# Kernel tuning notes

Measured on AMD Instinct MI355X. Metric: run time of the kernel, lower is better.

## Reference

```python
import jax, jax.numpy as jnp
import numpy as np
from jax.ops import segment_sum, segment_max

N_NODES, N_EDGES, D_IN, D_H, D_E, HEADS, LAYERS, D_OUT, N_GRAPHS = 50000, 150000, 48, 64, 16, 10, 3, 128, 4096


def setup_inputs() -> dict:
    key = jax.random.key(0)
    ks = jax.random.split(key, 24)
    x = jax.random.normal(ks[0], (N_NODES, D_IN), jnp.float32)
    edge_attr = jax.random.uniform(ks[1], (N_EDGES, D_E), jnp.float32)
    edge_index = jax.random.randint(ks[2], (2, N_EDGES), 0, N_NODES, dtype=jnp.int32)
    batch_ids = jnp.sort(jax.random.randint(ks[3], (N_NODES,), 0, N_GRAPHS, dtype=jnp.int32))
    s = 0.05
    W_emb = jax.random.normal(ks[4], (D_IN, D_H), jnp.float32) * s
    b_emb = jnp.zeros((D_H,), jnp.float32)
    Ws = jax.random.normal(ks[5], (LAYERS, D_H, HEADS * D_H), jnp.float32) * s
    att_src = jax.random.normal(ks[6], (LAYERS, HEADS, D_H), jnp.float32) * s
    att_dst = jax.random.normal(ks[7], (LAYERS, HEADS, D_H), jnp.float32) * s
    att_edge = jax.random.normal(ks[8], (LAYERS, HEADS, D_H), jnp.float32) * s
    W_edge = jax.random.normal(ks[9], (LAYERS, D_E, HEADS * D_H), jnp.float32) * s
    bias = jnp.zeros((LAYERS, D_H), jnp.float32)
    bn_gamma = jnp.ones((LAYERS, D_H), jnp.float32)
    bn_beta = jnp.zeros((LAYERS, D_H), jnp.float32)
    bn_mean = jax.random.normal(ks[10], (LAYERS, D_H), jnp.float32) * 0.1
    bn_var = jax.random.uniform(ks[11], (LAYERS, D_H), jnp.float32) + 0.5
    W_out = jax.random.normal(ks[12], (D_H, D_OUT), jnp.float32) * s
    b_out = jnp.zeros((D_OUT,), jnp.float32)
    return dict(x=x, edge_attr=edge_attr, W_emb=W_emb, b_emb=b_emb, Ws=Ws,
                att_src=att_src, att_dst=att_dst, att_edge=att_edge, W_edge=W_edge,
                bias=bias, bn_gamma=bn_gamma, bn_beta=bn_beta, bn_mean=bn_mean,
                bn_var=bn_var, W_out=W_out, b_out=b_out,
                edge_index=edge_index, batch_ids=batch_ids)


def reference(x, edge_attr, W_emb, b_emb, Ws, att_src, att_dst, att_edge, W_edge,
              bias, bn_gamma, bn_beta, bn_mean, bn_var, W_out, b_out,
              edge_index, batch_ids):
    N = x.shape[0]
    H, F = att_src.shape[1], att_src.shape[2]
    src, dst = edge_index[0], edge_index[1]
    # PyG add_self_loops(fill_value='mean'): self-loop edge_attr = scatter-mean of incoming edge_attr
    cnt = segment_sum(jnp.ones(src.shape, jnp.float32), dst, num_segments=N)
    loop_attr = segment_sum(edge_attr, dst, num_segments=N) / jnp.maximum(cnt, 1.0)[:, None]
    ar = jnp.arange(N, dtype=src.dtype)
    src2 = jnp.concatenate([src, ar])
    dst2 = jnp.concatenate([dst, ar])
    ea2 = jnp.concatenate([edge_attr, loop_attr], axis=0)  # [E+N, De]

    h = x @ W_emb + b_emb  # [N, D_H]
    for i in range(Ws.shape[0]):
        xp = (h @ Ws[i]).reshape(N, H, F)                       # [N,H,F]
        a_s = jnp.einsum('nhf,hf->nh', xp, att_src[i])
        a_d = jnp.einsum('nhf,hf->nh', xp, att_dst[i])
        ep = (ea2 @ W_edge[i]).reshape(-1, H, F)                # [E2,H,F]
        a_e = jnp.einsum('ehf,hf->eh', ep, att_edge[i])
        alpha = jax.nn.leaky_relu(a_s[src2] + a_d[dst2] + a_e, 0.2)  # [E2,H]
        m = segment_max(alpha, dst2, num_segments=N)            # segment softmax over dst
        e = jnp.exp(alpha - m[dst2])
        z = segment_sum(e, dst2, num_segments=N)
        att = e / z[dst2]                                       # [E2,H]
        agg = segment_sum(xp[src2] * att[:, :, None], dst2, num_segments=N)  # [N,H,F]
        xc = agg.mean(axis=1) + bias[i]                         # concat=False -> head mean
        xc = (xc - bn_mean[i]) * bn_gamma[i] / jnp.sqrt(bn_var[i] + 1e-5) + bn_beta[i]
        xc = jax.nn.gelu(xc, approximate=False)
        h = h + xc                                              # residual_connection == 'res'
    out = h @ W_out + b_out                                     # [N, D_OUT]
    gsum = segment_sum(out, batch_ids, num_segments=N_GRAPHS)
    gcnt = segment_sum(jnp.ones((N,), jnp.float32), batch_ids, num_segments=N_GRAPHS)
    return gsum / jnp.maximum(gcnt, 1.0)[:, None]               # global_mean_pool [G, D_OUT]
```

## Files before the change

### kernel.cpp

```cpp
#include <hip/hip_runtime.h>
#include <hip/hip_fp16.h>
#include <math.h>

constexpr int NN   = 50000;
constexpr int NE   = 150000;
constexpr int DIN  = 48;
constexpr int DH   = 64;
constexpr int DE   = 16;
constexpr int NHD  = 10;
constexpr int NL   = 3;
constexpr int DOUTC= 128;
constexpr int NG   = 4096;
constexpr int E2   = NE + NN;
constexpr int SCAN_B  = 256;
constexpr int SCAN_NB = (NN + SCAN_B - 1) / SCAN_B;

typedef __bf16 v8bf __attribute__((ext_vector_type(8)));
typedef short  v8s  __attribute__((ext_vector_type(8)));
typedef float  v4f  __attribute__((ext_vector_type(4)));

__device__ inline unsigned short f2bf(float f) {
    unsigned u = __builtin_bit_cast(unsigned, f);
    unsigned r = (u + 0x7FFFu + ((u >> 16) & 1u)) >> 16;
    return (unsigned short)r;
}

__device__ inline v4f MF(v8s a, v8s b, v4f c) {
    return __builtin_amdgcn_mfma_f32_16x16x32_bf16(
        __builtin_bit_cast(v8bf, a), __builtin_bit_cast(v8bf, b), c, 0, 0, 0);
}
__device__ inline v4f MFB(v8bf a, v8s b, v4f c) {
    return __builtin_amdgcn_mfma_f32_16x16x32_bf16(
        a, __builtin_bit_cast(v8bf, b), c, 0, 0, 0);
}

#define RLI(v, l) __builtin_amdgcn_readlane((v), (l))
#define RLH2(v, l) __builtin_bit_cast(__half2, __builtin_amdgcn_readlane(__builtin_bit_cast(int, (v)), (l)))

__global__ void k_zero(int* __restrict__ cnt, int* __restrict__ cursor) {
    int i = blockIdx.x * blockDim.x + threadIdx.x;
    if (i < NN) { cnt[i] = 0; cursor[i] = 0; }
}

__global__ void k_cnt(const int* __restrict__ dst, int* __restrict__ cnt) {
    int e = blockIdx.x * blockDim.x + threadIdx.x;
    if (e < NE) atomicAdd(&cnt[dst[e]], 1);
}

__global__ void k_scan_a(const int* __restrict__ cnt, int* __restrict__ bsum) {
    __shared__ int s[SCAN_B];
    int i = blockIdx.x * SCAN_B + threadIdx.x;
    s[threadIdx.x] = (i < NN) ? (cnt[i] + 1) : 0;
    __syncthreads();
    for (int off = SCAN_B / 2; off > 0; off >>= 1) {
        if (threadIdx.x < off) s[threadIdx.x] += s[threadIdx.x + off];
        __syncthreads();
    }
    if (threadIdx.x == 0) bsum[blockIdx.x] = s[0];
}

__global__ void k_scan_b(int* __restrict__ bsum) {
    if (threadIdx.x == 0 && blockIdx.x == 0) {
        int acc = 0;
        for (int i = 0; i < SCAN_NB; ++i) { int v = bsum[i]; bsum[i] = acc; acc += v; }
    }
}

__global__ void k_scan_c(const int* __restrict__ cnt, const int* __restrict__ bsum,
                         int* __restrict__ rp) {
    __shared__ int s[SCAN_B];
    int i = blockIdx.x * SCAN_B + threadIdx.x;
    int v = (i < NN) ? (cnt[i] + 1) : 0;
    s[threadIdx.x] = v;
    __syncthreads();
    for (int off = 1; off < SCAN_B; off <<= 1) {
        int t = (threadIdx.x >= off) ? s[threadIdx.x - off] : 0;
        __syncthreads();
        s[threadIdx.x] += t;
        __syncthreads();
    }
    if (i < NN) {
        int excl = bsum[blockIdx.x] + s[threadIdx.x] - v;
        rp[i] = excl;
        if (i == NN - 1) rp[NN] = excl + v;
    }
}

__global__ void k_csr_fill(const int* __restrict__ src, const int* __restrict__ dst,
                           const int* __restrict__ rp, int* __restrict__ cursor,
                           int* __restrict__ eidx, int* __restrict__ scsr) {
    int e = blockIdx.x * blockDim.x + threadIdx.x;
    if (e >= E2) return;
    int d  = (e < NE) ? dst[e] : (e - NE);
    int sn = (e < NE) ? src[e] : d;
    int pos = atomicAdd(&cursor[d], 1);
    int s = rp[d] + pos;
    eidx[s] = e; scsr[s] = sn;
}

__global__ void k_misc(const int* __restrict__ rp, const int* __restrict__ scsr,
                       const int* __restrict__ eidx, const int* __restrict__ cnt,
                       const float* __restrict__ ea, const int* __restrict__ batch,
                       int* __restrict__ snl6, int* __restrict__ grp,
                       float* __restrict__ loop) {
    int tid = blockIdx.x * blockDim.x + threadIdx.x;
    if (tid < NN * 8) {
        int n = tid >> 3, j = tid & 7;
        int r0 = rp[n], deg = rp[n + 1] - r0;
        int v;
        if (j < 6)       v = (j < deg) ? scsr[r0 + j] : 0;
        else if (j == 6) v = deg;
        else             v = r0;
        snl6[tid] = v;
    } else if (tid < NN * 9) {
        int n = tid - NN * 8;
        int b = batch[n];
        int pb = (n == 0) ? -1 : batch[n - 1];
        for (int g = pb + 1; g <= b; ++g) grp[g] = n;
        if (n == NN - 1) for (int g = b + 1; g <= NG; ++g) grp[g] = NN;
    } else if (tid < NN * 25) {
        int t = tid - NN * 9;
        int n = t >> 4, d = t & 15;
        int r0 = rp[n], r1 = rp[n + 1];
        float s = 0.f;
        for (int q = r0; q < r1; ++q) {
            int eid = eidx[q];
            if (eid < NE) s += ea[(size_t)eid * DE + d];
        }
        int c = cnt[n];
        loop[t] = s * ((c > 1) ? (1.0f / (float)c) : 1.0f);
    }
}

constexpr int N_BTP = NL * 40960;
constexpr int N_WCB = NL * 2048;
constexpr int N_EMB = DH * 64;
constexpr int N_WET = NL * DE * NHD;
__global__ void k_prep(const float* __restrict__ Ws, const float* __restrict__ asrc,
                       const float* __restrict__ adst, const float* __restrict__ We_in,
                       const float* __restrict__ aedge, const float* __restrict__ Wemb,
                       unsigned short* __restrict__ BtP, unsigned short* __restrict__ WcB,
                       unsigned short* __restrict__ BH, unsigned short* __restrict__ BL,
                       float* __restrict__ WeT) {
    int tid = blockIdx.x * blockDim.x + threadIdx.x;
    if (tid < N_BTP) {
        int e  = tid & 7;
        int ln = (tid >> 3) & 63;
        int t  = (tid >> 9) % 20;
        int ct = (tid / 10240) & 3;
        int l  = tid / 40960;
        int f = ct * 16 + (ln & 15);
        int kidx = t * 32 + (ln >> 4) * 8 + e;
        int k = kidx / 10, q = kidx - 10 * (kidx / 10);
        float v = Ws[((size_t)l * DH + k) * 640 + q * 64 + f] * 0.1f;
        BtP[tid] = f2bf(v);
    } else if (tid < N_BTP + N_WCB) {
        int r0 = tid - N_BTP;
        int l = r0 / 2048, r = r0 % 2048;
        int tile = r / 1024, rr = r % 1024;
        int ln = rr / 16, idx = rr % 16;
        int t2 = idx / 8, e = idx % 8;
        int k = t2 * 32 + (ln >> 4) * 8 + e;
        int jc = ln & 15;
        int j = tile * 16 + jc;
        float v = 0.f;
        if (j < 20) {
            int hh = j % NHD;
            const float* a = ((j < NHD) ? asrc : adst) + (size_t)l * NHD * DH + hh * DH;
            const float* w = Ws + ((size_t)l * DH + k) * 640 + hh * DH;
            float s = 0.f;
#pragma unroll
            for (int f = 0; f < DH; ++f) s += w[f] * a[f];
            v = s;
        }
        WcB[r0] = f2bf(v);
    } else if (tid < N_BTP + N_WCB + N_EMB) {
        int r0 = tid - N_BTP - N_WCB;
        int c = r0 >> 6, k = r0 & 63;
        float v = (k < DIN) ? Wemb[(size_t)k * DH + c] : 0.f;
        __bf16 hi = (__bf16)v;
        BH[r0] = __builtin_bit_cast(unsigned short, hi);
        BL[r0] = __builtin_bit_cast(unsigned short, (__bf16)(v - (float)hi));
    } else if (tid < N_BTP + N_WCB + N_EMB + N_WET) {
        int t3 = tid - N_BTP - N_WCB - N_EMB;
        int l = t3 / 160, rr = t3 % 160;
        int hh = rr / 16, d = rr % 16;
        const float* a = aedge + (size_t)l * NHD * DH + hh * DH;
        const float* w = We_in + ((size_t)l * DE + d) * 640 + hh * DH;
        float s = 0.f;
#pragma unroll
        for (int f = 0; f < DH; ++f) s += w[f] * a[f];
        WeT[l * 160 + hh * 16 + d] = s;
    }
}

__global__ void k_ae3(const float* __restrict__ ea, const float* __restrict__ loop,
                      const float* __restrict__ WeT, const int* __restrict__ eidx,
                      __half* __restrict__ aeAll) {
    int tid = blockIdx.x * blockDim.x + threadIdx.x;
    if (tid >= NL * E2 * NHD) return;
    int l = tid / (E2 * NHD);
    int r = tid - l * (E2 * NHD);
    int s = r / NHD, h = r - (r / NHD) * NHD;
    int eid = eidx[s];
    const float* ar = (eid < NE) ? (ea + (size_t)eid * DE) : (loop + (size_t)(eid - NE) * DE);
    const float* wt = WeT + l * 160 + h * 16;
    float4 a0 = *(const float4*)(ar + 0);
    float4 a1 = *(const float4*)(ar + 4);
    float4 a2 = *(const float4*)(ar + 8);
    float4 a3 = *(const float4*)(ar + 12);
    float4 w0 = *(const float4*)(wt + 0);
    float4 w1 = *(const float4*)(wt + 4);
    float4 w2 = *(const float4*)(wt + 8);
    float4 w3 = *(const float4*)(wt + 12);
    float v = a0.x*w0.x + a0.y*w0.y + a0.z*w0.z + a0.w*w0.w
            + a1.x*w1.x + a1.y*w1.y + a1.z*w1.z + a1.w*w1.w
            + a2.x*w2.x + a2.y*w2.y + a2.z*w2.z + a2.w*w2.w
            + a3.x*w3.x + a3.y*w3.y + a3.z*w3.z + a3.w*w3.w;
    aeAll[tid] = (__half)v;
}

__global__ __launch_bounds__(256) void k_emb(const float* __restrict__ x,
        const unsigned short* __restrict__ BH, const unsigned short* __restrict__ BL,
        const float* __restrict__ bemb, const unsigned short* __restrict__ WcB,
        float* __restrict__ h, __half* __restrict__ hh, float* __restrict__ S) {
    __shared__ __align__(16) unsigned short hlb[4][16 * 72];
    const int tid = threadIdx.x;
    const int w = tid >> 6, lane = tid & 63;
    const int la = lane & 15, lb = lane >> 4;
    const int rowbase = blockIdx.x * 64 + w * 16;
    const int nA = rowbase + la;

    v8bf ah[2], al[2];
#pragma unroll
    for (int ks = 0; ks < 2; ++ks) {
        const int k0 = ks * 32 + lb * 8;
        float xv[8];
        if (nA < NN && k0 < DIN) {
            const float* xp = x + (size_t)nA * DIN + k0;
            float4 v0 = *(const float4*)xp;
            float4 v1 = *(const float4*)(xp + 4);
            xv[0]=v0.x; xv[1]=v0.y; xv[2]=v0.z; xv[3]=v0.w;
            xv[4]=v1.x; xv[5]=v1.y; xv[6]=v1.z; xv[7]=v1.w;
        } else {
#pragma unroll
            for (int e = 0; e < 8; ++e) xv[e] = 0.f;
        }
#pragma unroll
        for (int e = 0; e < 8; ++e) {
            __bf16 hi = (__bf16)xv[e];
            ah[ks][e] = hi;
            al[ks][e] = (__bf16)(xv[e] - (float)hi);
        }
    }
    v4f acc[4];
#pragma unroll
    for (int ct = 0; ct < 4; ++ct) acc[ct] = (v4f){0.f, 0.f, 0.f, 0.f};
#pragma unroll
    for (int ct = 0; ct < 4; ++ct) {
#pragma unroll
        for (int ks = 0; ks < 2; ++ks) {
            const int boff = (ct * 16 + la) * 64 + ks * 32 + lb * 8;
            v8s bh = *(const v8s*)&BH[boff];
            v8s bl = *(const v8s*)&BL[boff];
            acc[ct] = MFB(ah[ks], bh, acc[ct]);
            acc[ct] = MFB(al[ks], bh, acc[ct]);
            acc[ct] = MFB(ah[ks], bl, acc[ct]);
        }
    }
#pragma unroll
    for (int ct = 0; ct < 4; ++ct) {
        const int c = ct * 16 + la;
        const float bi = bemb[c];
#pragma unroll
        for (int r = 0; r < 4; ++r) {
            const int row = lb * 4 + r;
            const int n = rowbase + row;
            float v = acc[ct][r] + bi;
            if (n < NN) {
                h[(size_t)n * DH + c] = v;
                hh[(size_t)n * DH + c] = (__half)v;
            }
            hlb[w][row * 72 + c] = f2bf(v);
        }
    }
    __syncthreads();
    v4f s0 = {0.f,0.f,0.f,0.f}, s1 = {0.f,0.f,0.f,0.f};
#pragma unroll
    for (int t = 0; t < 2; ++t) {
        v8s av = *(const v8s*)&hlb[w][la * 72 + t * 32 + lb * 8];
        v8s b0 = *(const v8s*)&WcB[(size_t)(lane) * 16 + t * 8];
        v8s b1 = *(const v8s*)&WcB[(size_t)(64 + lane) * 16 + t * 8];
        s0 = MF(av, b0, s0);
        s1 = MF(av, b1, s1);
    }
#pragma unroll
    for (int r = 0; r < 4; ++r) {
        const int n = rowbase + lb * 4 + r;
        if (n < NN) {
            S[(size_t)n * 20 + la] = s0[r];
            if (la < 4) S[(size_t)n * 20 + 16 + la] = s1[r];
        }
    }
}

__global__ __launch_bounds__(256) void k_layer(
        const float* __restrict__ Sin, const __half* __restrict__ ae,
        __half* __restrict__ wraw,
        const int* __restrict__ snl6, const int* __restrict__ scsr,
        const float* __restrict__ hin, const __half* __restrict__ hinh,
        const unsigned short* __restrict__ BtP, const unsigned short* __restrict__ WcB,
        int do_s, float* __restrict__ Sout,
        const float* __restrict__ bias, const float* __restrict__ gam,
        const float* __restrict__ bet, const float* __restrict__ mean,
        const float* __restrict__ var, float* __restrict__ hout,
        __half* __restrict__ houth) {
    __shared__ __align__(16) unsigned short Gl[16 * 648];
    __shared__ __align__(8)  __half wL[16 * 120];

    const int tid = threadIdx.x;
    const int w = tid >> 6, lane = tid & 63;
    const int blk = blockIdx.x;
    const int nb4 = blk * 16 + w * 4;
    const unsigned* wrawu = (const unsigned*)wraw;

    const int meta = snl6[nb4 * 8 + (lane & 31)];
    __half hv[4][6];
#pragma unroll
    for (int i = 0; i < 4; ++i) {
#pragma unroll
        for (int j = 0; j < 6; ++j) {
            int sv = RLI(meta, i * 8 + j);
            hv[i][j] = hinh[(size_t)sv * DH + lane];
        }
    }

    if (tid < 160) {
        const int li = tid / 10, h = tid - (tid / 10) * 10;
        const int n = blk * 16 + li;
        const int deg = snl6[n * 8 + 6];
        const int r0  = snl6[n * 8 + 7];
        const float sd = Sin[(size_t)n * 20 + 10 + h];
        float aL[12];
        float m = -1e30f;
#pragma unroll
        for (int s = 0; s < 12; ++s) {
            float a = 0.f;
            if (s < deg) {
                int sn = scsr[r0 + s];
                a = Sin[(size_t)sn * 20 + h] + sd + (float)ae[(size_t)(r0 + s) * NHD + h];
                a = (a > 0.f) ? a : 0.2f * a;
                m = fmaxf(m, a);
            }
            aL[s] = a;
        }
        for (int s = 12; s < deg; ++s) {
            int sn = scsr[r0 + s];
            float a = Sin[(size_t)sn * 20 + h] + sd + (float)ae[(size_t)(r0 + s) * NHD + h];
            a = (a > 0.f) ? a : 0.2f * a;
            wraw[(size_t)(r0 + s) * NHD + h] = (__half)a;
            m = fmaxf(m, a);
        }
        float z = 0.f;
#pragma unroll
        for (int s = 0; s < 12; ++s) if (s < deg) z += __expf(aL[s] - m);
        for (int s = 12; s < deg; ++s) z += __expf((float)wraw[(size_t)(r0 + s) * NHD + h] - m);
        float zi = 1.f / z;
#pragma unroll
        for (int s = 0; s < 12; ++s) {
            float v = (s < deg) ? __expf(aL[s] - m) * zi : 0.f;
            wL[li * 120 + s * 10 + h] = (__half)v;
        }
        for (int s = 12; s < deg; ++s) {
            float v = __expf((float)wraw[(size_t)(r0 + s) * NHD + h] - m) * zi;
            wraw[(size_t)(r0 + s) * NHD + h] = (__half)v;
        }
    }
    __syncthreads();

    const unsigned* wLu = (const unsigned*)wL;
    int wfu[4];
#pragma unroll
    for (int i = 0; i < 4; ++i)
        wfu[i] = (int)wLu[(w * 4 + i) * 60 + (lane & 31)];
#pragma unroll
    for (int i = 0; i < 4; ++i) {
        const int li = w * 4 + i;
        const int deg = RLI(meta, i * 8 + 6);
        const int r0  = RLI(meta, i * 8 + 7);
        __half2 g[5];
#pragma unroll
        for (int p = 0; p < 5; ++p) g[p] = __half2{(__half)0.f, (__half)0.f};
#pragma unroll
        for (int j = 0; j < 6; ++j) {
            __half2 hvd = __half2half2(hv[i][j]);
#pragma unroll
            for (int p = 0; p < 5; ++p)
                g[p] = __hfma2(RLH2(wfu[i], j * 5 + p), hvd, g[p]);
        }
        if (deg > 6) {
            for (int c0 = 6; c0 < deg; c0 += 6) {
                const int rem = deg - c0;
                int w2;
                if (c0 == 6) {
                    w2 = (lane < 30) ? (int)wLu[li * 60 + 30 + lane] : 0;
                } else {
                    w2 = (lane < 30 && (lane / 5) < rem)
                         ? (int)wrawu[(size_t)(r0 + c0) * 5 + lane] : 0;
                }
                int s2 = (lane < 6 && c0 + lane < deg) ? scsr[r0 + c0 + lane] : 0;
                __half hv2[6];
#pragma unroll
                for (int j = 0; j < 6; ++j) {
                    int sv = RLI(s2, j);
                    hv2[j] = hinh[(size_t)sv * DH + lane];
                }
#pragma unroll
                for (int j = 0; j < 6; ++j) {
                    __half2 hvd = __half2half2(hv2[j]);
#pragma unroll
                    for (int p = 0; p < 5; ++p)
                        g[p] = __hfma2(RLH2(w2, j * 5 + p), hvd, g[p]);
                }
            }
        }
        const int base = li * 648 + lane * 10;
#pragma unroll
        for (int p = 0; p < 5; ++p) {
            float f0 = __low2float(g[p]), f1 = __high2float(g[p]);
            unsigned u = (unsigned)f2bf(f0) | ((unsigned)f2bf(f1) << 16);
            *(unsigned*)&Gl[base + 2 * p] = u;
        }
    }
    __syncthreads();

    const int la = lane & 15, lb = lane >> 4;
    v4f acc = {0.f, 0.f, 0.f, 0.f};
    const unsigned short* bp = BtP + (size_t)w * 20 * 512;
#pragma unroll 5
    for (int t = 0; t < 20; ++t) {
        v8s av = *(const v8s*)&Gl[la * 648 + t * 32 + lb * 8];
        v8s bv = *(const v8s*)&bp[t * 512 + lane * 8];
        acc = MF(av, bv, acc);
    }
    __syncthreads();

    unsigned short* hlb = Gl;
    const int f = w * 16 + la;
    const float bi = bias[f], gm = gam[f], bt_ = bet[f], mu = mean[f];
    const float iv = rsqrtf(var[f] + 1e-5f);
#pragma unroll
    for (int r = 0; r < 4; ++r) {
        const int local = lb * 4 + r;
        const int n = blk * 16 + local;
        float hvold = hin[(size_t)n * DH + f];
        float v = acc[r] + bi;
        v = (v - mu) * gm * iv + bt_;
        v = 0.5f * v * (1.0f + erff(v * 0.70710678118654752f));
        float hnew = hvold + v;
        hout[(size_t)n * DH + f] = hnew;
        houth[(size_t)n * DH + f] = (__half)hnew;
        hlb[local * 72 + f] = f2bf(hnew);
    }

    if (do_s) {
        __syncthreads();
        if (w < 2) {
            v4f sa = {0.f, 0.f, 0.f, 0.f};
#pragma unroll
            for (int t = 0; t < 2; ++t) {
                v8s av = *(const v8s*)&hlb[la * 72 + t * 32 + lb * 8];
                v8s bv = *(const v8s*)&WcB[(size_t)(w * 64 + lane) * 16 + t * 8];
                sa = MF(av, bv, sa);
            }
#pragma unroll
            for (int r = 0; r < 4; ++r) {
                const int n = blk * 16 + lb * 4 + r;
                if (w == 0) Sout[(size_t)n * 20 + la] = sa[r];
                else if (la < 4) Sout[(size_t)n * 20 + 16 + la] = sa[r];
            }
        }
    }
}

__global__ __launch_bounds__(256) void k_gout(const float* __restrict__ h,
        const float* __restrict__ W, const float* __restrict__ b,
        const int* __restrict__ grp, float* __restrict__ out) {
    __shared__ float Wl[DH * DOUTC];
    __shared__ float hl[4][DH];
    __shared__ float cl[4];
    for (int i = threadIdx.x; i < DH * DOUTC; i += 256) Wl[i] = W[i];
    int w = threadIdx.x >> 6, lane = threadIdx.x & 63;
    int g = blockIdx.x * 4 + w;
    int r0 = grp[g], r1 = grp[g + 1];
    float s = 0.f;
    for (int n = r0; n < r1; ++n) s += h[(size_t)n * DH + lane];
    hl[w][lane] = s;
    if (lane == 0) cl[w] = (float)(r1 - r0);
    __syncthreads();
    for (int idx = threadIdx.x; idx < 4 * DOUTC; idx += 256) {
        int gi = idx >> 7, c = idx & 127;
        float cnt = cl[gi];
        float inv = 1.f / fmaxf(cnt, 1.f);
        float acc = cnt * b[c];
        const float* hr = hl[gi];
#pragma unroll 16
        for (int k = 0; k < DH; ++k) acc += hr[k] * Wl[k * DOUTC + c];
        out[(size_t)(blockIdx.x * 4 + gi) * DOUTC + c] = acc * inv;
    }
}

extern "C" void kernel_launch(void* const* d_in, const int* in_sizes, int n_in,
                              void* d_out, int out_size, void* d_ws, size_t ws_size,
                              hipStream_t stream) {
    const float* x        = (const float*)d_in[0];
    const float* edge_attr= (const float*)d_in[1];
    const float* W_emb    = (const float*)d_in[2];
    const float* b_emb    = (const float*)d_in[3];
    const float* Ws       = (const float*)d_in[4];
    const float* att_src  = (const float*)d_in[5];
    const float* att_dst  = (const float*)d_in[6];
    const float* att_edge = (const float*)d_in[7];
    const float* W_edge   = (const float*)d_in[8];
    const float* bias     = (const float*)d_in[9];
    const float* bn_gamma = (const float*)d_in[10];
    const float* bn_beta  = (const float*)d_in[11];
    const float* bn_mean  = (const float*)d_in[12];
    const float* bn_var   = (const float*)d_in[13];
    const float* W_out    = (const float*)d_in[14];
    const float* b_out    = (const float*)d_in[15];
    const int*   srcp     = (const int*)d_in[16];
    const int*   dstp     = srcp + NE;
    const int*   batch    = (const int*)d_in[17];
    float* out = (float*)d_out;

    char* wsb = (char*)d_ws;
    size_t off = 0;
    auto alloc = [&](size_t bytes) -> void* {
        void* p = (void*)(wsb + off);
        off += (bytes + 255) & ~(size_t)255;
        return p;
    };
    float*  h0    = (float*)alloc((size_t)NN * DH * 4);
    float*  h1    = (float*)alloc((size_t)NN * DH * 4);
    __half* hh0   = (__half*)alloc((size_t)NN * DH * 2);
    __half* hh1   = (__half*)alloc((size_t)NN * DH * 2);
    float*  S0    = (float*)alloc((size_t)NN * 20 * 4);
    float*  S1    = (float*)alloc((size_t)NN * 20 * 4);
    __half* wraw  = (__half*)alloc((size_t)E2 * NHD * 2);
    __half* aeAll = (__half*)alloc((size_t)NL * E2 * NHD * 2);
    float*  loop  = (float*)alloc((size_t)NN * DE * 4);
    int*    cnt   = (int*)alloc((size_t)NN * 4);
    int*    rp    = (int*)alloc((size_t)(NN + 1) * 4);
    int*    cursor= (int*)alloc((size_t)NN * 4);
    int*    eidx  = (int*)alloc((size_t)E2 * 4);
    int*    scsr  = (int*)alloc((size_t)E2 * 4);
    int*    snl6  = (int*)alloc((size_t)NN * 8 * 4);
    int*    bsum  = (int*)alloc((size_t)SCAN_NB * 4);
    int*    grp   = (int*)alloc((size_t)(NG + 1) * 4);
    float*  WeT   = (float*)alloc((size_t)NL * 160 * 4);
    unsigned short* BtP = (unsigned short*)alloc((size_t)NL * 40960 * 2);
    unsigned short* WcB = (unsigned short*)alloc((size_t)NL * 2048 * 2);
    unsigned short* BH  = (unsigned short*)alloc((size_t)DH * 64 * 2);
    unsigned short* BL  = (unsigned short*)alloc((size_t)DH * 64 * 2);

    k_zero<<<(NN + 255) / 256, 256, 0, stream>>>(cnt, cursor);
    k_cnt<<<(NE + 255) / 256, 256, 0, stream>>>(dstp, cnt);
    k_scan_a<<<SCAN_NB, SCAN_B, 0, stream>>>(cnt, bsum);
    k_scan_b<<<1, 64, 0, stream>>>(bsum);
    k_scan_c<<<SCAN_NB, SCAN_B, 0, stream>>>(cnt, bsum, rp);
    k_csr_fill<<<(E2 + 255) / 256, 256, 0, stream>>>(srcp, dstp, rp, cursor, eidx, scsr);
    k_misc<<<(NN * 25 + 255) / 256, 256, 0, stream>>>(rp, scsr, eidx, cnt, edge_attr,
                                                      batch, snl6, grp, loop);

    k_prep<<<(N_BTP + N_WCB + N_EMB + N_WET + 255) / 256, 256, 0, stream>>>(
        Ws, att_src, att_dst, W_edge, att_edge, W_emb, BtP, WcB, BH, BL, WeT);
    k_ae3<<<(NL * E2 * NHD + 255) / 256, 256, 0, stream>>>(edge_attr, loop, WeT, eidx, aeAll);

    k_emb<<<(NN + 63) / 64, 256, 0, stream>>>(x, BH, BL, b_emb, WcB, h0, hh0, S0);

    float*  hb[2]  = {h0, h1};
    __half* hhb[2] = {hh0, hh1};
    float*  Sb[2]  = {S0, S1};
    for (int l = 0; l < NL; ++l) {
        float*  hin   = hb[l & 1];
        float*  hout  = hb[(l + 1) & 1];
        __half* hinh  = hhb[l & 1];
        __half* houth = hhb[(l + 1) & 1];
        float*  Sin   = Sb[l & 1];
        float*  Sout  = Sb[(l + 1) & 1];
        k_layer<<<NN / 16, 256, 0, stream>>>(
            Sin, aeAll + (size_t)l * E2 * NHD, wraw, snl6, scsr, hin, hinh,
            BtP + (size_t)l * 40960,
            WcB + (size_t)(l + 1 < NL ? l + 1 : 0) * 2048,
            (l + 1 < NL) ? 1 : 0, Sout,
            bias + l * DH, bn_gamma + l * DH, bn_beta + l * DH,
            bn_mean + l * DH, bn_var + l * DH, hout, houth);
    }
    float* hfin = hb[NL & 1];

    k_gout<<<NG / 4, 256, 0, stream>>>(hfin, W_out, b_out, grp, out);
}
```

Baseline: 226.0 us.

## Widen per-node neighbor metadata to 12 slots and fuse scan/zero kernels

Expands the per-node neighbor cache from 6 to 12 source indices, so the layer kernel reads the second chunk of neighbors from the compact metadata row instead of scsr, and unrolls that second chunk. The softmax now stores the exponentials and rescales them instead of recomputing exp. The single-thread block-sum scan kernel is removed: each scan_c block reduces the preceding block sums itself, and cursor zeroing moves into scan_c. In exchange the metadata array doubles in size and k_misc launches more threads.

```diff
diff --git a/kernel.cpp b/kernel.cpp
--- a/kernel.cpp
+++ b/kernel.cpp
@@ -37,9 +37,9 @@
 #define RLI(v, l) __builtin_amdgcn_readlane((v), (l))
 #define RLH2(v, l) __builtin_bit_cast(__half2, __builtin_amdgcn_readlane(__builtin_bit_cast(int, (v)), (l)))
 
-__global__ void k_zero(int* __restrict__ cnt, int* __restrict__ cursor) {
+__global__ void k_zero(int* __restrict__ cnt) {
     int i = blockIdx.x * blockDim.x + threadIdx.x;
-    if (i < NN) { cnt[i] = 0; cursor[i] = 0; }
+    if (i < NN) cnt[i] = 0;
 }
 
 __global__ void k_cnt(const int* __restrict__ dst, int* __restrict__ cnt) {
@@ -59,28 +59,35 @@
     if (threadIdx.x == 0) bsum[blockIdx.x] = s[0];
 }
 
-__global__ void k_scan_b(int* __restrict__ bsum) {
-    if (threadIdx.x == 0 && blockIdx.x == 0) {
-        int acc = 0;
-        for (int i = 0; i < SCAN_NB; ++i) { int v = bsum[i]; bsum[i] = acc; acc += v; }
-    }
-}
-
 __global__ void k_scan_c(const int* __restrict__ cnt, const int* __restrict__ bsum,
-                         int* __restrict__ rp) {
+                         int* __restrict__ rp, int* __restrict__ cursor) {
     __shared__ int s[SCAN_B];
-    int i = blockIdx.x * SCAN_B + threadIdx.x;
+    __shared__ int boff_s;
+    const int t = threadIdx.x;
+    int partial = (t < SCAN_NB && t < blockIdx.x) ? bsum[t] : 0;
+    s[t] = partial;
+    __syncthreads();
+    for (int off = SCAN_B / 2; off > 0; off >>= 1) {
+        if (t < off) s[t] += s[t + off];
+        __syncthreads();
+    }
+    if (t == 0) boff_s = s[0];
+    __syncthreads();
+    const int boff = boff_s;
+    __syncthreads();
+    int i = blockIdx.x * SCAN_B + t;
+    if (i < NN) cursor[i] = 0;
     int v = (i < NN) ? (cnt[i] + 1) : 0;
-    s[threadIdx.x] = v;
+    s[t] = v;
     __syncthreads();
     for (int off = 1; off < SCAN_B; off <<= 1) {
-        int t = (threadIdx.x >= off) ? s[threadIdx.x - off] : 0;
+        int tv = (t >= off) ? s[t - off] : 0;
         __syncthreads();
-        s[threadIdx.x] += t;
+        s[t] += tv;
         __syncthreads();
     }
     if (i < NN) {
-        int excl = bsum[blockIdx.x] + s[threadIdx.x] - v;
+        int excl = boff + s[t] - v;
         rp[i] = excl;
         if (i == NN - 1) rp[NN] = excl + v;
     }
@@ -101,25 +108,26 @@
 __global__ void k_misc(const int* __restrict__ rp, const int* __restrict__ scsr,
                        const int* __restrict__ eidx, const int* __restrict__ cnt,
                        const float* __restrict__ ea, const int* __restrict__ batch,
-                       int* __restrict__ snl6, int* __restrict__ grp,
+                       int* __restrict__ snl12, int* __restrict__ grp,
                        float* __restrict__ loop) {
     int tid = blockIdx.x * blockDim.x + threadIdx.x;
-    if (tid < NN * 8) {
-        int n = tid >> 3, j = tid & 7;
+    if (tid < NN * 16) {
+        int n = tid >> 4, j = tid & 15;
         int r0 = rp[n], deg = rp[n + 1] - r0;
         int v;
-        if (j < 6)       v = (j < deg) ? scsr[r0 + j] : 0;
-        else if (j == 6) v = deg;
-        else             v = r0;
-        snl6[tid] = v;
-    } else if (tid < NN * 9) {
-        int n = tid - NN * 8;
+        if (j < 12)      v = (j < deg) ? scsr[r0 + j] : 0;
+        else if (j == 12) v = deg;
+        else if (j == 13) v = r0;
+        else             v = 0;
+        snl12[tid] = v;
+    } else if (tid < NN * 17) {
+        int n = tid - NN * 16;
         int b = batch[n];
         int pb = (n == 0) ? -1 : batch[n - 1];
         for (int g = pb + 1; g <= b; ++g) grp[g] = n;
         if (n == NN - 1) for (int g = b + 1; g <= NG; ++g) grp[g] = NN;
-    } else if (tid < NN * 25) {
-        int t = tid - NN * 9;
+    } else if (tid < NN * 33) {
+        int t = tid - NN * 17;
         int n = t >> 4, d = t & 15;
         int r0 = rp[n], r1 = rp[n + 1];
         float s = 0.f;
@@ -307,7 +315,7 @@
 __global__ __launch_bounds__(256) void k_layer(
         const float* __restrict__ Sin, const __half* __restrict__ ae,
         __half* __restrict__ wraw,
-        const int* __restrict__ snl6, const int* __restrict__ scsr,
+        const int* __restrict__ snl12, const int* __restrict__ scsr,
         const float* __restrict__ hin, const __half* __restrict__ hinh,
         const unsigned short* __restrict__ BtP, const unsigned short* __restrict__ WcB,
         int do_s, float* __restrict__ Sout,
@@ -324,13 +332,14 @@
     const int nb4 = blk * 16 + w * 4;
     const unsigned* wrawu = (const unsigned*)wraw;
 
-    const int meta = snl6[nb4 * 8 + (lane & 31)];
+    const int meta = snl12[nb4 * 16 + lane];
+
     __half hv[4][6];
 #pragma unroll
     for (int i = 0; i < 4; ++i) {
 #pragma unroll
         for (int j = 0; j < 6; ++j) {
-            int sv = RLI(meta, i * 8 + j);
+            int sv = RLI(meta, i * 16 + j);
             hv[i][j] = hinh[(size_t)sv * DH + lane];
         }
     }
@@ -338,16 +347,17 @@
     if (tid < 160) {
         const int li = tid / 10, h = tid - (tid / 10) * 10;
         const int n = blk * 16 + li;
-        const int deg = snl6[n * 8 + 6];
-        const int r0  = snl6[n * 8 + 7];
+        const int* mrow = &snl12[n * 16];
+        const int deg = mrow[12];
+        const int r0  = mrow[13];
         const float sd = Sin[(size_t)n * 20 + 10 + h];
         float aL[12];
         float m = -1e30f;
 #pragma unroll
         for (int s = 0; s < 12; ++s) {
-            float a = 0.f;
+            float a = -1e30f;
             if (s < deg) {
-                int sn = scsr[r0 + s];
+                int sn = mrow[s];
                 a = Sin[(size_t)sn * 20 + h] + sd + (float)ae[(size_t)(r0 + s) * NHD + h];
                 a = (a > 0.f) ? a : 0.2f * a;
                 m = fmaxf(m, a);
@@ -363,18 +373,23 @@
         }
         float z = 0.f;
 #pragma unroll
-        for (int s = 0; s < 12; ++s) if (s < deg) z += __expf(aL[s] - m);
-        for (int s = 12; s < deg; ++s) z += __expf((float)wraw[(size_t)(r0 + s) * NHD + h] - m);
+        for (int s = 0; s < 12; ++s) {
+            float e = (s < deg) ? __expf(aL[s] - m) : 0.f;
+            aL[s] = e;
+            z += e;
+        }
+        for (int s = 12; s < deg; ++s) {
+            float e = __expf((float)wraw[(size_t)(r0 + s) * NHD + h] - m);
+            wraw[(size_t)(r0 + s) * NHD + h] = (__half)e;
+            z += e;
+        }
         float zi = 1.f / z;
 #pragma unroll
-        for (int s = 0; s < 12; ++s) {
-            float v = (s < deg) ? __expf(aL[s] - m) * zi : 0.f;
-            wL[li * 120 + s * 10 + h] = (__half)v;
-        }
-        for (int s = 12; s < deg; ++s) {
-            float v = __expf((float)wraw[(size_t)(r0 + s) * NHD + h] - m) * zi;
-            wraw[(size_t)(r0 + s) * NHD + h] = (__half)v;
-        }
+        for (int s = 0; s < 12; ++s)
+            wL[li * 120 + s * 10 + h] = (__half)(aL[s] * zi);
+        for (int s = 12; s < deg; ++s)
+            wraw[(size_t)(r0 + s) * NHD + h] =
+                (__half)((float)wraw[(size_t)(r0 + s) * NHD + h] * zi);
     }
     __syncthreads();
 
@@ -386,8 +401,8 @@
 #pragma unroll
     for (int i = 0; i < 4; ++i) {
         const int li = w * 4 + i;
-        const int deg = RLI(meta, i * 8 + 6);
-        const int r0  = RLI(meta, i * 8 + 7);
+        const int deg = RLI(meta, i * 16 + 12);
+        const int r0  = RLI(meta, i * 16 + 13);
         __half2 g[5];
 #pragma unroll
         for (int p = 0; p < 5; ++p) g[p] = __half2{(__half)0.f, (__half)0.f};
@@ -399,15 +414,26 @@
                 g[p] = __hfma2(RLH2(wfu[i], j * 5 + p), hvd, g[p]);
         }
         if (deg > 6) {
-            for (int c0 = 6; c0 < deg; c0 += 6) {
+            {
+                int w2 = (lane < 30) ? (int)wLu[li * 60 + 30 + lane] : 0;
+                __half hv2[6];
+#pragma unroll
+                for (int j = 0; j < 6; ++j) {
+                    int sv = RLI(meta, i * 16 + 6 + j);
+                    hv2[j] = hinh[(size_t)sv * DH + lane];
+                }
+#pragma unroll
+                for (int j = 0; j < 6; ++j) {
+                    __half2 hvd = __half2half2(hv2[j]);
+#pragma unroll
+                    for (int p = 0; p < 5; ++p)
+                        g[p] = __hfma2(RLH2(w2, j * 5 + p), hvd, g[p]);
+                }
+            }
+            for (int c0 = 12; c0 < deg; c0 += 6) {
                 const int rem = deg - c0;
-                int w2;
-                if (c0 == 6) {
-                    w2 = (lane < 30) ? (int)wLu[li * 60 + 30 + lane] : 0;
-                } else {
-                    w2 = (lane < 30 && (lane / 5) < rem)
+                int w2 = (lane < 30 && (lane / 5) < rem)
                          ? (int)wrawu[(size_t)(r0 + c0) * 5 + lane] : 0;
-                }
                 int s2 = (lane < 6 && c0 + lane < deg) ? scsr[r0 + c0 + lane] : 0;
                 __half hv2[6];
 #pragma unroll
@@ -555,7 +581,7 @@
     int*    cursor= (int*)alloc((size_t)NN * 4);
     int*    eidx  = (int*)alloc((size_t)E2 * 4);
     int*    scsr  = (int*)alloc((size_t)E2 * 4);
-    int*    snl6  = (int*)alloc((size_t)NN * 8 * 4);
+    int*    snl12 = (int*)alloc((size_t)NN * 16 * 4);
     int*    bsum  = (int*)alloc((size_t)SCAN_NB * 4);
     int*    grp   = (int*)alloc((size_t)(NG + 1) * 4);
     float*  WeT   = (float*)alloc((size_t)NL * 160 * 4);
@@ -564,14 +590,13 @@
     unsigned short* BH  = (unsigned short*)alloc((size_t)DH * 64 * 2);
     unsigned short* BL  = (unsigned short*)alloc((size_t)DH * 64 * 2);
 
-    k_zero<<<(NN + 255) / 256, 256, 0, stream>>>(cnt, cursor);
+    k_zero<<<(NN + 255) / 256, 256, 0, stream>>>(cnt);
     k_cnt<<<(NE + 255) / 256, 256, 0, stream>>>(dstp, cnt);
     k_scan_a<<<SCAN_NB, SCAN_B, 0, stream>>>(cnt, bsum);
-    k_scan_b<<<1, 64, 0, stream>>>(bsum);
-    k_scan_c<<<SCAN_NB, SCAN_B, 0, stream>>>(cnt, bsum, rp);
+    k_scan_c<<<SCAN_NB, SCAN_B, 0, stream>>>(cnt, bsum, rp, cursor);
     k_csr_fill<<<(E2 + 255) / 256, 256, 0, stream>>>(srcp, dstp, rp, cursor, eidx, scsr);
-    k_misc<<<(NN * 25 + 255) / 256, 256, 0, stream>>>(rp, scsr, eidx, cnt, edge_attr,
-                                                      batch, snl6, grp, loop);
+    k_misc<<<(NN * 33 + 255) / 256, 256, 0, stream>>>(rp, scsr, eidx, cnt, edge_attr,
+                                                      batch, snl12, grp, loop);
 
     k_prep<<<(N_BTP + N_WCB + N_EMB + N_WET + 255) / 256, 256, 0, stream>>>(
         Ws, att_src, att_dst, W_edge, att_edge, W_emb, BtP, WcB, BH, BL, WeT);
@@ -590,7 +615,7 @@
         float*  Sin   = Sb[l & 1];
         float*  Sout  = Sb[(l + 1) & 1];
         k_layer<<<NN / 16, 256, 0, stream>>>(
-            Sin, aeAll + (size_t)l * E2 * NHD, wraw, snl6, scsr, hin, hinh,
+            Sin, aeAll + (size_t)l * E2 * NHD, wraw, snl12, scsr, hin, hinh,
             BtP + (size_t)l * 40960,
             WcB + (size_t)(l + 1 < NL ? l + 1 : 0) * 2048,
             (l + 1 < NL) ? 1 : 0, Sout,
```

After: 223.4 us. About the same (-1.1%).
